# Optimization experiments

Hardware: AMD Instinct MI355X
Metric: run time of the kernel (lower is better)

Reference implementation:

```python
import jax, jax.numpy as jnp
import numpy as np

B, C, H, W = 4, 64, 160, 160
OUT, KH, KW = 64, 3, 3
STRIDE, PAD = 1, 1
K2 = KH * KW


def conv2d(x, w, b=None, stride=STRIDE, pad=PAD):
    y = jax.lax.conv_general_dilated(
        x, w, window_strides=(stride, stride),
        padding=[(pad, pad), (pad, pad)],
        dimension_numbers=("NCHW", "OIHW", "NCHW"))
    if b is not None:
        y = y + b[None, :, None, None]
    return y


def bilinear_gather(x, py, px):
    # x: [B,C,H,W]; py,px: [B,K2,Ho,Wo] float sampling positions
    Bq, Cq, Hq, Wq = x.shape
    y0 = jnp.floor(py)
    x0 = jnp.floor(px)
    wy1 = py - y0  # frac
    wx1 = px - x0
    y0i = y0.astype(jnp.int32)
    x0i = x0.astype(jnp.int32)
    x_flat = x.reshape(Bq, Cq, Hq * Wq)

    def corner(yi, xi, wgt):
        valid = (yi >= 0) & (yi < Hq) & (xi >= 0) & (xi < Wq)
        idx = jnp.clip(yi, 0, Hq - 1) * Wq + jnp.clip(xi, 0, Wq - 1)  # [B,K2,Ho,Wo]
        g = jax.vmap(lambda xf, i: jnp.take(xf, i, axis=1))(x_flat, idx)  # [B,C,K2,Ho,Wo]
        return g * (wgt * valid)[:, None]

    out = corner(y0i, x0i, (1 - wy1) * (1 - wx1))
    out = out + corner(y0i, x0i + 1, (1 - wy1) * wx1)
    out = out + corner(y0i + 1, x0i, wy1 * (1 - wx1))
    out = out + corner(y0i + 1, x0i + 1, wy1 * wx1)
    return out  # [B,C,K2,Ho,Wo]


def deform_forward(x, offset_w, offset_b, mask_w, mask_b, dcn_w):
    offset = conv2d(x, offset_w, offset_b)                # [B, 2*K2, Ho, Wo]
    mask = jax.nn.sigmoid(conv2d(x, mask_w, mask_b))      # [B, K2, Ho, Wo]
    Bq, _, Ho, Wo = offset.shape
    off = offset.reshape(Bq, K2, 2, Ho, Wo)
    off_y, off_x = off[:, :, 0], off[:, :, 1]
    k = jnp.arange(K2)
    ky = (k // KW).astype(jnp.float32)
    kx = (k % KW).astype(jnp.float32)
    base_i = jnp.arange(Ho, dtype=jnp.float32) * STRIDE - PAD
    base_j = jnp.arange(Wo, dtype=jnp.float32) * STRIDE - PAD
    py = off_y + base_i[None, None, :, None] + ky[None, :, None, None]
    px = off_x + base_j[None, None, None, :] + kx[None, :, None, None]
    sampled = bilinear_gather(x, py, px)                  # [B,C,K2,Ho,Wo]
    w = dcn_w.reshape(OUT, C, K2)
    # out[b,o,i,j] = sum_{c,k} w[o,c,k] * mask[b,k,i,j] * sampled[b,c,k,i,j]
    return jnp.einsum("ock,bckij,bkij->boij", w, sampled, mask)


def setup_inputs() -> dict:
    key = jax.random.key(0)
    ks = jax.random.split(key, 6)
    x = jax.random.normal(ks[0], (B, C, H, W), dtype=jnp.float32)
    # small random weights so offsets stay modest (module inits them to 0;
    # random values exercise the full deformable math)
    offset_w = jax.random.normal(ks[1], (2 * K2, C, KH, KW), dtype=jnp.float32) * 0.01
    offset_b = jax.random.normal(ks[2], (2 * K2,), dtype=jnp.float32) * 0.1
    mask_w = jax.random.normal(ks[3], (K2, C, KH, KW), dtype=jnp.float32) * 0.01
    mask_b = jax.random.normal(ks[4], (K2,), dtype=jnp.float32) * 0.1
    dcn_w = jax.random.normal(ks[5], (OUT, C, KH, KW), dtype=jnp.float32) * (1.0 / np.sqrt(C * K2))
    return {"x": x, "offset_w": offset_w, "offset_b": offset_b,
            "mask_w": mask_w, "mask_b": mask_b, "dcn_w": dcn_w}


def reference(x, offset_w, offset_b, mask_w, mask_b, dcn_w):
    return deform_forward(x, offset_w, offset_b, mask_w, mask_b, dcn_w)
```

## Files before the change

kernel.cpp:

```cpp
#include <hip/hip_runtime.h>
#include <math.h>

#define Bq 4
#define Cq 64
#define Hq 160
#define Wq 160
#define HWq (Hq*Wq)
#define OUTq 64
#define KKq 576
#define KS  18
#define SROW 584
#define HSTRIDE 72

typedef __attribute__((ext_vector_type(8))) _Float16 half8;
typedef __attribute__((ext_vector_type(2))) _Float16 half2v;
typedef __attribute__((ext_vector_type(4))) float float4v;
typedef __attribute__((ext_vector_type(4))) unsigned short ushort4v;
typedef unsigned short ushort_t;
typedef unsigned int uint_t;

__device__ __forceinline__ ushort_t f2h(float f) {
    return __builtin_bit_cast(ushort_t, (_Float16)f);
}
__device__ __forceinline__ uint_t f2hdup(float f) {
    uint_t u = (uint_t)f2h(f);
    return u | (u << 16);
}
__device__ __forceinline__ half2v h2(uint_t u) {
    return __builtin_bit_cast(half2v, u);
}
#define MFMA16(a,b,c) __builtin_amdgcn_mfma_f32_16x16x32_f16((a),(b),(c),0,0,0)

__global__ void __launch_bounds__(256) k_prep(const float* __restrict__ x,
                                              const float* __restrict__ dcn_w,
                                              const float* __restrict__ off_w,
                                              const float* __restrict__ msk_w,
                                              ushort_t* __restrict__ xt,
                                              ushort_t* __restrict__ wtf,
                                              ushort_t* __restrict__ cwf2) {
    __shared__ float tile[64][65];
    int b = blockIdx.y, hw0 = blockIdx.x * 64;
    int tid = threadIdx.x;
    int l16 = tid & 15, crow = tid >> 4;
#pragma unroll
    for (int i = 0; i < 4; ++i) {
        int c = crow + i*16;
        float4 v = *(const float4*)(x + ((size_t)(b*Cq + c))*HWq + hw0 + l16*4);
        tile[c][l16*4+0] = v.x;
        tile[c][l16*4+1] = v.y;
        tile[c][l16*4+2] = v.z;
        tile[c][l16*4+3] = v.w;
    }
    __syncthreads();
#pragma unroll
    for (int it = 0; it < 4; ++it) {
        int hw = (tid >> 4) + it*16;
        int c4 = (tid & 15) * 4;
        uint_t v0 = (uint_t)f2h(tile[c4+0][hw]) | ((uint_t)f2h(tile[c4+1][hw]) << 16);
        uint_t v1 = (uint_t)f2h(tile[c4+2][hw]) | ((uint_t)f2h(tile[c4+3][hw]) << 16);
        uint2 vv; vv.x = v0; vv.y = v1;
        *(uint2*)(xt + ((size_t)b*HWq + hw0 + hw)*64 + c4) = vv;
    }
    if (blockIdx.y == 0 && blockIdx.x < 216) {
        int id = blockIdx.x*256 + tid;
        if (id < 4*KS*512) {
            int j = id & 7, ln = (id>>3) & 63, ks = (id>>9) % KS, g = id/(512*KS);
            int kk = ks*32 + (ln>>4)*8 + j;
            int c  = kk & 63, kt = kk >> 6;
            int m  = g*16 + (ln&15);
            wtf[id] = f2h(dcn_w[m*KKq + c*9 + kt]);
        }
        int id2 = id - 4*KS*512;
        if (id2 >= 0 && id2 < 9*2*2*512) {
            int j = id2 & 7, ln = (id2>>3) & 63;
            int ks2 = (id2>>9) & 1, g = (id2>>10) & 1, k = id2 >> 11;
            int co = g*16 + (ln&15);
            int c  = ks2*32 + (ln>>4)*8 + j;
            float w = 0.f;
            if (co < 18)      w = off_w[co*KKq + c*9 + k];
            else if (co < 27) w = msk_w[(co-18)*KKq + c*9 + k];
            cwf2[id2] = f2h(w);
        }
    }
}

__global__ void __launch_bounds__(256, 6) k_fused(const ushort_t* __restrict__ xt,
                                                  const ushort_t* __restrict__ cwf2,
                                                  const float* __restrict__ off_b,
                                                  const float* __restrict__ msk_b,
                                                  const ushort_t* __restrict__ wtf,
                                                  float* __restrict__ out) {
    __shared__ __align__(16) char s_mem[16*SROW*2];
    __shared__ __align__(16) ushort4v s_A16[144];
    __shared__ __align__(16) uint4 s_W[144];
    ushort_t* halo   = (ushort_t*)s_mem;
    float*    s_part = (float*)(s_mem + 7776);
    ushort_t* s_s    = (ushort_t*)s_mem;

    int bid = blockIdx.x;
    int blk = (bid & 7) * 800 + (bid >> 3);
    int jt = blk % 10, i = (blk/10) % Hq, b = blk/(10*Hq);
    int j0 = jt*16;
    int tid = threadIdx.x, lane = tid & 63, grp = tid >> 6;
    int n = lane & 15, quad = lane >> 4;

    int gM = grp & 1, kh = grp >> 1;
    half8 af[9];
#pragma unroll
    for (int s = 0; s < 9; ++s) {
        int st = kh*9 + s;
        int k = st >> 1, ks2 = st & 1;
        af[s] = *(const half8*)(cwf2 + (size_t)(((k*2+gM)*2+ks2)*512 + lane*8));
    }

    const ushort_t* xtb = xt + (size_t)b*HWq*64;
#pragma unroll
    for (int t = tid; t < 432; t += 256) {
        int seg = t >> 3, sub = t & 7;
        int ky = seg / 18, px = seg % 18;
        int y = i + ky - 1, xx = j0 + px - 1;
        uint4 v = {0u,0u,0u,0u};
        if (y >= 0 && y < Hq && xx >= 0 && xx < Wq)
            v = *(const uint4*)(xtb + ((size_t)y*Wq + xx)*64 + sub*8);
        *(uint4*)(halo + (ky*18 + px)*HSTRIDE + sub*8) = v;
    }
    __syncthreads();

    {
        float4v cacc = {0.f,0.f,0.f,0.f};
#pragma unroll
        for (int s = 0; s < 9; ++s) {
            int st = kh*9 + s;
            int k = st >> 1, ks2 = st & 1;
            int ky = k/3, kx = k - (k/3)*3;
            half8 bf = *(const half8*)(halo + (ky*18 + n + kx)*HSTRIDE + quad*8 + ks2*32);
            cacc = MFMA16(af[s], bf, cacc);
        }
        *(float4v*)(s_part + grp*256 + lane*4) = cacc;
    }
    __syncthreads();

    if (tid < 144) {
        int p = tid & 15, k = tid >> 4;
        #define RD(co) (s_part[(((co)>>4)*256)     + ((((co)&15)>>2)*16 + p)*4 + ((co)&3)] + \
                        s_part[(2 + ((co)>>4))*256 + ((((co)&15)>>2)*16 + p)*4 + ((co)&3)])
        float oy = RD(2*k)   + off_b[2*k];
        float ox = RD(2*k+1) + off_b[2*k+1];
        float mv = RD(18+k)  + msk_b[k];
        #undef RD
        float m = 1.f/(1.f + __expf(-mv));
        float py = oy + (float)(i - 1 + k/3);
        float px = ox + (float)(j0 + p - 1 + (k - (k/3)*3));
        float fy = floorf(py), fx = floorf(px);
        int y0 = (int)fy, x0 = (int)fx;
        float wy1 = py - fy, wx1 = px - fx;
        float wy0 = 1.f - wy1, wx0 = 1.f - wx1;
        bool vy0 = (y0 >= 0) & (y0 < Hq),   vy1 = (y0+1 >= 0) & (y0+1 < Hq);
        bool vx0 = (x0 >= 0) & (x0 < Wq),   vx1 = (x0+1 >= 0) & (x0+1 < Wq);
        int yc0 = min(max(y0,   0), Hq-1), yc1 = min(max(y0+1, 0), Hq-1);
        int xc0 = min(max(x0,   0), Wq-1), xc1 = min(max(x0+1, 0), Wq-1);
        ushort4v av;
        av.x = (ushort_t)(yc0*Wq + xc0);
        av.y = (ushort_t)(yc0*Wq + xc1);
        av.z = (ushort_t)(yc1*Wq + xc0);
        av.w = (ushort_t)(yc1*Wq + xc1);
        s_A16[tid] = av;
        s_W[tid] = make_uint4(f2hdup((vy0 && vx0) ? wy0*wx0*m : 0.f),
                              f2hdup((vy0 && vx1) ? wy0*wx1*m : 0.f),
                              f2hdup((vy1 && vx0) ? wy1*wx0*m : 0.f),
                              f2hdup((vy1 && vx1) ? wy1*wx1*m : 0.f));
    }
    __syncthreads();

    {
        int lane4 = (lane & 31) * 4;
        int halfi = lane >> 5;
        const char* xtbB = (const char*)xtb;
        char* s_sb = (char*)s_s;
        int t2h = grp*2 + halfi;
        ushort4v A = s_A16[t2h];
        uint4 Wt   = s_W[t2h];
        uint_t u00 = *(const uint_t*)(xtbB + (((uint_t)A.x) << 7) + lane4);
        uint_t u01 = *(const uint_t*)(xtbB + (((uint_t)A.y) << 7) + lane4);
        uint_t u10 = *(const uint_t*)(xtbB + (((uint_t)A.z) << 7) + lane4);
        uint_t u11 = *(const uint_t*)(xtbB + (((uint_t)A.w) << 7) + lane4);
#pragma unroll
        for (int iter = 0; iter < 18; ++iter) {
            int t_cur = t2h;
            uint4 Wc = Wt;
            uint_t v00 = u00, v01 = u01, v10 = u10, v11 = u11;
            if (iter < 17) {
                t2h += 8;
                A  = s_A16[t2h];
                Wt = s_W[t2h];
                u00 = *(const uint_t*)(xtbB + (((uint_t)A.x) << 7) + lane4);
                u01 = *(const uint_t*)(xtbB + (((uint_t)A.y) << 7) + lane4);
                u10 = *(const uint_t*)(xtbB + (((uint_t)A.z) << 7) + lane4);
                u11 = *(const uint_t*)(xtbB + (((uint_t)A.w) << 7) + lane4);
            }
            uint_t dst = (uint_t)((t_cur & 15)*(SROW*2) + (t_cur >> 4)*128);
            half2v acc2 = h2(v00) * h2(Wc.x);
            acc2 = __builtin_elementwise_fma(h2(v01), h2(Wc.y), acc2);
            acc2 = __builtin_elementwise_fma(h2(v10), h2(Wc.z), acc2);
            acc2 = __builtin_elementwise_fma(h2(v11), h2(Wc.w), acc2);
            *(uint_t*)(s_sb + dst + lane4) = __builtin_bit_cast(uint_t, acc2);
        }
    }
    __syncthreads();

    float4v acc = {0.f,0.f,0.f,0.f};
    const ushort_t* arow = wtf + ((size_t)(grp*KS)*64 + lane)*8;
    const ushort_t* brow = s_s + n*SROW + quad*8;
    half8 a_cur = *(const half8*)(arow);
#pragma unroll
    for (int ks = 0; ks < KS; ++ks) {
        half8 a_next = a_cur;
        if (ks < KS-1) a_next = *(const half8*)(arow + (ks+1)*512);
        half8 bf = *(const half8*)(brow + ks*32);
        acc = MFMA16(a_cur, bf, acc);
        a_cur = a_next;
    }

#pragma unroll
    for (int r = 0; r < 4; ++r) {
        int o = grp*16 + quad*4 + r;
        out[(((size_t)b*OUTq + o)*Hq + i)*Wq + j0 + n] = acc[r];
    }
}

extern "C" void kernel_launch(void* const* d_in, const int* in_sizes, int n_in,
                              void* d_out, int out_size, void* d_ws, size_t ws_size,
                              hipStream_t stream) {
    const float* x     = (const float*)d_in[0];
    const float* off_w = (const float*)d_in[1];
    const float* off_b = (const float*)d_in[2];
    const float* msk_w = (const float*)d_in[3];
    const float* msk_b = (const float*)d_in[4];
    const float* dcn_w = (const float*)d_in[5];
    float* out = (float*)d_out;

    char* ws = (char*)d_ws;
    ushort_t* xt   = (ushort_t*)ws;
    ushort_t* wtf  = xt + (size_t)Bq*HWq*64;
    ushort_t* cwf2 = wtf + 4*KS*512;

    hipLaunchKernelGGL(k_prep, dim3(HWq/64, Bq), dim3(256), 0, stream,
                       x, dcn_w, off_w, msk_w, xt, wtf, cwf2);
    hipLaunchKernelGGL(k_fused, dim3(Bq*Hq*10), dim3(256), 0, stream,
                       xt, cwf2, off_b, msk_b, wtf, out);
}
```

Before: 127.0 us.

## Process two output rows per block with 512 threads to share halo

Each block now computes two adjacent output rows (32 pixels) using 512 threads. It loads a 4-row halo instead of two separate 3-row halos, so the rows share the overlapping input. The offset/mask conv, bilinear sampling and final MFMA GEMM are all re-indexed for the doubled tile. This cuts halo global loads and per-block fixed overhead, but the larger blocks use more LDS and may lower occupancy (launch bounds 512,6 is likely unattainable).

Measured after the change: 131.3 us. 1.03x slower.

```diff
diff --git a/kernel.cpp b/kernel.cpp
--- a/kernel.cpp
+++ b/kernel.cpp
@@ -84,27 +84,28 @@
     }
 }
 
-__global__ void __launch_bounds__(256, 6) k_fused(const ushort_t* __restrict__ xt,
+__global__ void __launch_bounds__(512, 6) k_fused(const ushort_t* __restrict__ xt,
                                                   const ushort_t* __restrict__ cwf2,
                                                   const float* __restrict__ off_b,
                                                   const float* __restrict__ msk_b,
                                                   const ushort_t* __restrict__ wtf,
                                                   float* __restrict__ out) {
-    __shared__ __align__(16) char s_mem[16*SROW*2];
-    __shared__ __align__(16) ushort4v s_A16[144];
-    __shared__ __align__(16) uint4 s_W[144];
+    __shared__ __align__(16) char s_mem[32*SROW*2];
+    __shared__ __align__(16) ushort4v s_A16[288];
+    __shared__ __align__(16) uint4 s_W[288];
     ushort_t* halo   = (ushort_t*)s_mem;
-    float*    s_part = (float*)(s_mem + 7776);
+    float*    s_part = (float*)(s_mem + 10368);
     ushort_t* s_s    = (ushort_t*)s_mem;
 
     int bid = blockIdx.x;
-    int blk = (bid & 7) * 800 + (bid >> 3);
-    int jt = blk % 10, i = (blk/10) % Hq, b = blk/(10*Hq);
-    int j0 = jt*16;
-    int tid = threadIdx.x, lane = tid & 63, grp = tid >> 6;
+    int blk = (bid & 7) * 400 + (bid >> 3);
+    int jt = blk % 10, ih = (blk/10) % 80, b = blk/800;
+    int i = ih*2, j0 = jt*16;
+    int tid = threadIdx.x, lane = tid & 63, w = tid >> 6;
     int n = lane & 15, quad = lane >> 4;
 
-    int gM = grp & 1, kh = grp >> 1;
+    int gM = w & 1, kh = (w >> 1) & 1, r2 = w >> 2;
+
     half8 af[9];
 #pragma unroll
     for (int s = 0; s < 9; ++s) {
@@ -114,15 +115,27 @@
     }
 
     const ushort_t* xtb = xt + (size_t)b*HWq*64;
-#pragma unroll
-    for (int t = tid; t < 432; t += 256) {
-        int seg = t >> 3, sub = t & 7;
-        int ky = seg / 18, px = seg % 18;
-        int y = i + ky - 1, xx = j0 + px - 1;
-        uint4 v = {0u,0u,0u,0u};
-        if (y >= 0 && y < Hq && xx >= 0 && xx < Wq)
-            v = *(const uint4*)(xtb + ((size_t)y*Wq + xx)*64 + sub*8);
-        *(uint4*)(halo + (ky*18 + px)*HSTRIDE + sub*8) = v;
+    {
+        int t = tid;
+        {
+            int seg = t >> 3, sub = t & 7;
+            int hr = seg / 18, px = seg % 18;
+            int y = i + hr - 1, xx = j0 + px - 1;
+            uint4 v = {0u,0u,0u,0u};
+            if ((unsigned)y < (unsigned)Hq && (unsigned)xx < (unsigned)Wq)
+                v = *(const uint4*)(xtb + ((size_t)y*Wq + xx)*64 + sub*8);
+            *(uint4*)(halo + (hr*18 + px)*HSTRIDE + sub*8) = v;
+        }
+        t = tid + 512;
+        if (t < 576) {
+            int seg = t >> 3, sub = t & 7;
+            int hr = seg / 18, px = seg % 18;
+            int y = i + hr - 1, xx = j0 + px - 1;
+            uint4 v = {0u,0u,0u,0u};
+            if ((unsigned)y < (unsigned)Hq && (unsigned)xx < (unsigned)Wq)
+                v = *(const uint4*)(xtb + ((size_t)y*Wq + xx)*64 + sub*8);
+            *(uint4*)(halo + (hr*18 + px)*HSTRIDE + sub*8) = v;
+        }
     }
     __syncthreads();
 
@@ -133,23 +146,23 @@
             int st = kh*9 + s;
             int k = st >> 1, ks2 = st & 1;
             int ky = k/3, kx = k - (k/3)*3;
-            half8 bf = *(const half8*)(halo + (ky*18 + n + kx)*HSTRIDE + quad*8 + ks2*32);
+            half8 bf = *(const half8*)(halo + ((r2+ky)*18 + n + kx)*HSTRIDE + quad*8 + ks2*32);
             cacc = MFMA16(af[s], bf, cacc);
         }
-        *(float4v*)(s_part + grp*256 + lane*4) = cacc;
-    }
-    __syncthreads();
-
-    if (tid < 144) {
-        int p = tid & 15, k = tid >> 4;
-        #define RD(co) (s_part[(((co)>>4)*256)     + ((((co)&15)>>2)*16 + p)*4 + ((co)&3)] + \
-                        s_part[(2 + ((co)>>4))*256 + ((((co)&15)>>2)*16 + p)*4 + ((co)&3)])
+        *(float4v*)(s_part + w*256 + lane*4) = cacc;
+    }
+    __syncthreads();
+
+    if (tid < 288) {
+        int p = tid & 15, r = (tid >> 4) & 1, k = tid >> 5;
+        #define RD(co) (s_part[((r*4)     + ((co)>>4))*256 + ((((co)&15)>>2)*16 + p)*4 + ((co)&3)] + \
+                        s_part[((r*4) + 2 + ((co)>>4))*256 + ((((co)&15)>>2)*16 + p)*4 + ((co)&3)])
         float oy = RD(2*k)   + off_b[2*k];
         float ox = RD(2*k+1) + off_b[2*k+1];
         float mv = RD(18+k)  + msk_b[k];
         #undef RD
         float m = 1.f/(1.f + __expf(-mv));
-        float py = oy + (float)(i - 1 + k/3);
+        float py = oy + (float)(i + r - 1 + k/3);
         float px = ox + (float)(j0 + p - 1 + (k - (k/3)*3));
         float fy = floorf(py), fx = floorf(px);
         int y0 = (int)fy, x0 = (int)fx;
@@ -177,28 +190,28 @@
         int halfi = lane >> 5;
         const char* xtbB = (const char*)xtb;
         char* s_sb = (char*)s_s;
-        int t2h = grp*2 + halfi;
-        ushort4v A = s_A16[t2h];
-        uint4 Wt   = s_W[t2h];
+        int t = w*2 + halfi;
+        ushort4v A = s_A16[t];
+        uint4 Wt   = s_W[t];
         uint_t u00 = *(const uint_t*)(xtbB + (((uint_t)A.x) << 7) + lane4);
         uint_t u01 = *(const uint_t*)(xtbB + (((uint_t)A.y) << 7) + lane4);
         uint_t u10 = *(const uint_t*)(xtbB + (((uint_t)A.z) << 7) + lane4);
         uint_t u11 = *(const uint_t*)(xtbB + (((uint_t)A.w) << 7) + lane4);
 #pragma unroll
         for (int iter = 0; iter < 18; ++iter) {
-            int t_cur = t2h;
+            int t_cur = t;
             uint4 Wc = Wt;
             uint_t v00 = u00, v01 = u01, v10 = u10, v11 = u11;
             if (iter < 17) {
-                t2h += 8;
-                A  = s_A16[t2h];
-                Wt = s_W[t2h];
+                t += 16;
+                A  = s_A16[t];
+                Wt = s_W[t];
                 u00 = *(const uint_t*)(xtbB + (((uint_t)A.x) << 7) + lane4);
                 u01 = *(const uint_t*)(xtbB + (((uint_t)A.y) << 7) + lane4);
                 u10 = *(const uint_t*)(xtbB + (((uint_t)A.z) << 7) + lane4);
                 u11 = *(const uint_t*)(xtbB + (((uint_t)A.w) << 7) + lane4);
             }
-            uint_t dst = (uint_t)((t_cur & 15)*(SROW*2) + (t_cur >> 4)*128);
+            uint_t dst = (uint_t)((t_cur & 31)*(SROW*2) + (t_cur >> 5)*128);
             half2v acc2 = h2(v00) * h2(Wc.x);
             acc2 = __builtin_elementwise_fma(h2(v01), h2(Wc.y), acc2);
             acc2 = __builtin_elementwise_fma(h2(v10), h2(Wc.z), acc2);
@@ -208,23 +221,25 @@
     }
     __syncthreads();
 
-    float4v acc = {0.f,0.f,0.f,0.f};
-    const ushort_t* arow = wtf + ((size_t)(grp*KS)*64 + lane)*8;
-    const ushort_t* brow = s_s + n*SROW + quad*8;
-    half8 a_cur = *(const half8*)(arow);
-#pragma unroll
-    for (int ks = 0; ks < KS; ++ks) {
-        half8 a_next = a_cur;
-        if (ks < KS-1) a_next = *(const half8*)(arow + (ks+1)*512);
-        half8 bf = *(const half8*)(brow + ks*32);
-        acc = MFMA16(a_cur, bf, acc);
-        a_cur = a_next;
-    }
-
-#pragma unroll
-    for (int r = 0; r < 4; ++r) {
-        int o = grp*16 + quad*4 + r;
-        out[(((size_t)b*OUTq + o)*Hq + i)*Wq + j0 + n] = acc[r];
+    {
+        int g = w >> 1, nt = w & 1;
+        float4v acc = {0.f,0.f,0.f,0.f};
+        const ushort_t* arow = wtf + ((size_t)(g*KS)*64 + lane)*8;
+        const ushort_t* brow = s_s + (nt*16 + n)*SROW + quad*8;
+        half8 a_cur = *(const half8*)(arow);
+#pragma unroll
+        for (int ks = 0; ks < KS; ++ks) {
+            half8 a_next = a_cur;
+            if (ks < KS-1) a_next = *(const half8*)(arow + (ks+1)*512);
+            half8 bf = *(const half8*)(brow + ks*32);
+            acc = MFMA16(a_cur, bf, acc);
+            a_cur = a_next;
+        }
+#pragma unroll
+        for (int rr = 0; rr < 4; ++rr) {
+            int o = g*16 + quad*4 + rr;
+            out[(((size_t)b*OUTq + o)*Hq + (i + nt))*Wq + j0 + n] = acc[rr];
+        }
     }
 }
 
@@ -246,6 +261,6 @@
 
     hipLaunchKernelGGL(k_prep, dim3(HWq/64, Bq), dim3(256), 0, stream,
                        x, dcn_w, off_w, msk_w, xt, wtf, cwf2);
-    hipLaunchKernelGGL(k_fused, dim3(Bq*Hq*10), dim3(256), 0, stream,
+    hipLaunchKernelGGL(k_fused, dim3(Bq*Hq*10/2), dim3(512), 0, stream,
                        xt, cwf2, off_b, msk_b, wtf, out);
 }
```
